# Optimization experiments

Measured on AMD Instinct MI355X. Metric: run time of the kernel, lower is better.

The kernel has to match this reference:

```python
import jax, jax.numpy as jnp
import numpy as np

B, CIN, H, W = 4, 64, 160, 160
G, K = 8, 3
KK = K * K
PAD = K // 2
CG = CIN // G  # channels per deformable group


def setup_inputs() -> dict:
    key = jax.random.key(0)
    ks = jax.random.split(key, 6)
    x = jax.random.normal(ks[0], (B, CIN, H, W), jnp.float32)
    feat = jax.random.normal(ks[1], (B, CIN, H, W), jnp.float32)
    # conv_offset weights (zero-init in the original; small random here so offsets are nontrivial)
    w_off = jax.random.normal(ks[2], (3 * G * KK, CIN, 3, 3), jnp.float32) * 0.01
    b_off = jax.random.normal(ks[3], (3 * G * KK,), jnp.float32) * 0.01
    # deformable conv weights (torchvision DeformConv2d: groups=1, bias=True)
    w_dcn = jax.random.normal(ks[4], (CIN, CIN, K, K), jnp.float32) * (1.0 / np.sqrt(CIN * KK))
    b_dcn = jax.random.normal(ks[5], (CIN,), jnp.float32) * 0.01
    return dict(x=x, feat=feat, w_off=w_off, b_off=b_off, w_dcn=w_dcn, b_dcn=b_dcn)


def _modulated_deform_conv(x, offset, mask, w, b):
    # x: [B,C,H,W]; offset: [B,2*G*KK,H,W] (interleaved dy,dx per (g,k));
    # mask: [B,G*KK,H,W]; w: [Cout,C,K,K]; stride 1, zero padding K//2.
    Bn, C, Hh, Ww = x.shape
    off = offset.reshape(Bn, G, KK, 2, Hh, Ww)
    dy = off[:, :, :, 0]  # [B,G,KK,H,W]
    dx = off[:, :, :, 1]
    ki = jnp.arange(K)
    base_y = (jnp.repeat(ki, K) - PAD).reshape(1, 1, KK, 1, 1).astype(x.dtype)
    base_x = (jnp.tile(ki, K) - PAD).reshape(1, 1, KK, 1, 1).astype(x.dtype)
    hy = jnp.arange(Hh, dtype=x.dtype).reshape(1, 1, 1, Hh, 1)
    wx = jnp.arange(Ww, dtype=x.dtype).reshape(1, 1, 1, 1, Ww)
    py = hy + base_y + dy  # sample rows  [B,G,KK,H,W]
    px = wx + base_x + dx  # sample cols
    y0 = jnp.floor(py)
    x0 = jnp.floor(px)
    ly = py - y0
    lx = px - x0
    y0i = y0.astype(jnp.int32)
    x0i = x0.astype(jnp.int32)
    xg = x.reshape(Bn, G, CG, Hh * Ww)

    def gather(yi, xi):
        valid = ((yi >= 0) & (yi < Hh) & (xi >= 0) & (xi < Ww)).astype(x.dtype)
        idx = jnp.clip(yi, 0, Hh - 1) * Ww + jnp.clip(xi, 0, Ww - 1)
        flat = idx.reshape(Bn, G, 1, KK * Hh * Ww)
        v = jnp.take_along_axis(xg, flat, axis=3).reshape(Bn, G, CG, KK, Hh, Ww)
        return v * valid[:, :, None]  # zero padding outside

    v = ((1 - ly) * (1 - lx))[:, :, None] * gather(y0i, x0i) \
      + ((1 - ly) * lx)[:, :, None] * gather(y0i, x0i + 1) \
      + (ly * (1 - lx))[:, :, None] * gather(y0i + 1, x0i) \
      + (ly * lx)[:, :, None] * gather(y0i + 1, x0i + 1)
    v = v * mask.reshape(Bn, G, 1, KK, Hh, Ww)
    wr = w.reshape(w.shape[0], G, CG, KK)
    out = jnp.einsum('ogck,bgckhw->bohw', wr, v) + b[None, :, None, None]
    return out


def reference(x, feat, w_off, b_off, w_dcn, b_dcn):
    # conv_offset: 3x3 conv, stride 1, pad 1
    out = jax.lax.conv_general_dilated(
        feat, w_off, (1, 1), ((1, 1), (1, 1)),
        dimension_numbers=('NCHW', 'OIHW', 'NCHW')) + b_off[None, :, None, None]
    o1, o2, m = jnp.split(out, 3, axis=1)
    offset = jnp.concatenate([o1, o2], axis=1)  # [B, 2*G*KK, H, W]
    mask = jax.nn.sigmoid(m)                    # [B, G*KK, H, W]
    return _modulated_deform_conv(x, offset, mask, w_dcn, b_dcn)
```

## Files before the change

kernel.cpp:

```cpp
#include <hip/hip_runtime.h>
#include <math.h>

#define Bn   4
#define CINc 64
#define Hh   160
#define Ww   160
#define Gg   8
#define HW   (Hh * Ww)
#define COFF 216

#define OROW 220
#define VROW 200
#define OFFS_SZ (64 * OROW)
#define UNION_SZ 12800

typedef short bf16x8 __attribute__((ext_vector_type(8)));
typedef float f32x4  __attribute__((ext_vector_type(4)));

static __device__ __forceinline__ unsigned short f2bf(float f) {
    unsigned int u = __float_as_uint(f);
    u = (u + 0x7fffu + ((u >> 16) & 1u)) >> 16;
    return (unsigned short)u;
}
static __device__ __forceinline__ float bf2f(unsigned short s) {
    return __uint_as_float(((unsigned int)s) << 16);
}
static __device__ __forceinline__ float blo(unsigned int u) {
    return __uint_as_float(u << 16);
}
static __device__ __forceinline__ float bhi(unsigned int u) {
    return __uint_as_float(u & 0xffff0000u);
}

#define WB 180
__global__ __launch_bounds__(256)
void prep_kernel(const float* __restrict__ feat, const float* __restrict__ x,
                 const float* __restrict__ w_off, const float* __restrict__ w_dcn,
                 unsigned short* __restrict__ featT, unsigned short* __restrict__ xG,
                 unsigned short* __restrict__ wofrag, unsigned short* __restrict__ wfrag) {
    const int blk = blockIdx.x;
    const int t = threadIdx.x;
    if (blk < 1280) {
        __shared__ float tile[CINc][161];
        const int isx = blk >= 640;
        const int rem = isx ? blk - 640 : blk;
        const int b = rem / Hh;
        const int h = rem % Hh;
        const float* src = isx ? x : feat;
        for (int i = t; i < CINc * Ww; i += 256) {
            int ci = i / Ww, w = i % Ww;
            tile[ci][w] = src[(((size_t)b * CINc + ci) * Hh + h) * Ww + w];
        }
        __syncthreads();
        if (isx) {
            for (int i = t; i < CINc * Ww; i += 256) {
                int g = i / (Ww * 8);
                int r = i % (Ww * 8);
                int w = r >> 3, cg = r & 7;
                xG[(((size_t)b * Gg + g) * HW + h * Ww + w) * 8 + cg] = f2bf(tile[g * 8 + cg][w]);
            }
        } else {
            for (int i = t; i < CINc * Ww; i += 256) {
                int w = i / CINc, ci = i % CINc;
                featT[(((size_t)b * Hh + h) * Ww + w) * CINc + ci] = f2bf(tile[ci][w]);
            }
        }
    } else {
        for (int e = (blk - 1280) * 256 + t; e < 147456 + 36864; e += WB * 256) {
            if (e < 147456) {
                const int j    = e & 7;
                const int lane = (e >> 3) & 63;
                const int rest = e >> 9;
                const int mt = rest & 15;
                const int q  = rest >> 4;
                const int ks = q & 1;
                const int kp = q >> 1;
                const int co = mt * 16 + (lane & 15);
                const int ci = ks * 32 + (lane >> 4) * 8 + j;
                float v = (co < COFF) ? w_off[(size_t)co * 576 + ci * 9 + kp] : 0.f;
                wofrag[e] = f2bf(v);
            } else {
                const int e2   = e - 147456;
                const int j    = e2 & 7;
                const int lane = (e2 >> 3) & 63;
                const int mt   = (e2 >> 9) & 3;
                const int ks   = e2 >> 11;
                const int m = mt * 16 + (lane & 15);
                const int k = ks * 32 + (lane >> 4) * 8 + j;
                const int g = k / 72, r = k % 72;
                const int kk = r >> 3, cg = r & 7;
                const int ci = g * 8 + cg;
                wfrag[e2] = f2bf(w_dcn[((size_t)m * CINc + ci) * 9 + kk]);
            }
        }
    }
}

__global__ __launch_bounds__(256, 3)
void dcnpack_fused(const unsigned short* __restrict__ featT,
                   const unsigned short* __restrict__ xG,
                   const unsigned short* __restrict__ wofrag,
                   const unsigned short* __restrict__ wfrag,
                   const float* __restrict__ b_off,
                   const float* __restrict__ b_dcn,
                   float* __restrict__ out) {
    __shared__ unsigned short smem[OFFS_SZ + UNION_SZ];
    unsigned short* offs = smem;
    unsigned short* halo = smem + OFFS_SZ;
    unsigned short* vbuf = smem + OFFS_SZ;

    const int b  = blockIdx.z;
    const int h0 = blockIdx.y * 8;
    const int w0 = blockIdx.x * 8;
    const int t  = threadIdx.x;
    const int wv   = t >> 6;
    const int lane = t & 63;
    const int n    = lane & 15;
    const int kg   = lane >> 4;

    for (int task = t; task < 800; task += 256) {
        const int pix = task >> 3, ch = task & 7;
        const int ry = pix / 10, rx = pix % 10;
        const int gh = h0 - 1 + ry, gw = w0 - 1 + rx;
        float4 v = make_float4(0.f, 0.f, 0.f, 0.f);
        if (gh >= 0 && gh < Hh && gw >= 0 && gw < Ww)
            v = *(const float4*)(featT + ((((size_t)b * Hh) + gh) * Ww + gw) * CINc + ch * 8);
        *(float4*)(halo + pix * 72 + ch * 8) = v;
    }
    __syncthreads();

    const int bbase0 = (((n >> 3) * 10) + (n & 7)) * 72 + kg * 8;

    f32x4 cacc[4][4] = {};
    #pragma unroll
    for (int s = 0; s < 18; ++s) {
        const int kp = s >> 1, ks = s & 1;
        const int ky = kp / 3, kx = kp % 3;
        bf16x8 af[4];
        #pragma unroll
        for (int i = 0; i < 4; ++i)
            af[i] = *(const bf16x8*)(wofrag +
                (((size_t)(kp * 2 + ks) * 16 + wv + 4 * i) * 64 + lane) * 8);
        #pragma unroll
        for (int nt = 0; nt < 4; ++nt) {
            const bf16x8 bfr = *(const bf16x8*)(halo + bbase0 + nt * 1440 +
                                                (ky * 10 + kx) * 72 + ks * 32);
            #pragma unroll
            for (int i = 0; i < 4; ++i)
                cacc[i][nt] = __builtin_amdgcn_mfma_f32_16x16x32_bf16(af[i], bfr, cacc[i][nt], 0, 0, 0);
        }
    }

    #pragma unroll
    for (int i = 0; i < 4; ++i) {
        const int mt = wv + 4 * i;
        #pragma unroll
        for (int r = 0; r < 4; ++r) {
            const int co = mt * 16 + kg * 4 + r;
            if (co < COFF) {
                const float bias = b_off[co];
                const int ismask = (co >= 144);
                const int gk = ismask ? (co - 144) : (co >> 1);
                const int type = ismask ? 2 : (co & 1);
                #pragma unroll
                for (int nt = 0; nt < 4; ++nt) {
                    const int p = nt * 16 + n;
                    float v = cacc[i][nt][r] + bias;
                    if (ismask) v = 1.f / (1.f + expf(-v));
                    offs[p * OROW + gk * 3 + type] = f2bf(v);
                }
            }
        }
    }
    __syncthreads();

    f32x4 dacc[4] = {};

    for (int c = 0; c < 3; ++c) {
        #pragma unroll 3
        for (int it = 0; it < 6; ++it) {
            const int task = t + it * 256;
            const int p    = task & 63;
            const int u    = c * 24 + (task >> 6);
            const int g    = u / 9;
            const int k    = u % 9;
            const int h = h0 + (p >> 3);
            const int w = w0 + (p & 7);

            const float dy   = bf2f(offs[p * OROW + u * 3 + 0]);
            const float dx   = bf2f(offs[p * OROW + u * 3 + 1]);
            const float mask = bf2f(offs[p * OROW + u * 3 + 2]);

            const float py  = (float)h + (float)(k / 3 - 1) + dy;
            const float pxx = (float)w + (float)(k % 3 - 1) + dx;
            const float y0f = floorf(py), x0f = floorf(pxx);
            const float ly = py - y0f, lx = pxx - x0f;
            const int y0 = (int)y0f, x0i = (int)x0f;
            const int y1 = y0 + 1,  x1  = x0i + 1;

            const float vy0 = (y0 >= 0 && y0 < Hh) ? 1.f : 0.f;
            const float vy1 = (y1 >= 0 && y1 < Hh) ? 1.f : 0.f;
            const float vx0 = (x0i >= 0 && x0i < Ww) ? 1.f : 0.f;
            const float vx1 = (x1 >= 0 && x1 < Ww) ? 1.f : 0.f;

            const float c00 = (1.f - ly) * (1.f - lx) * vy0 * vx0 * mask;
            const float c01 = (1.f - ly) * lx         * vy0 * vx1 * mask;
            const float c10 = ly         * (1.f - lx) * vy1 * vx0 * mask;
            const float c11 = ly         * lx         * vy1 * vx1 * mask;

            const int y0c = min(max(y0, 0), Hh - 1), y1c = min(max(y1, 0), Hh - 1);
            const int x0c = min(max(x0i, 0), Ww - 1), x1c = min(max(x1, 0), Ww - 1);

            const unsigned short* xb = xG + ((size_t)b * Gg + g) * HW * 8;
            const uint4 q00 = *(const uint4*)(xb + ((size_t)y0c * Ww + x0c) * 8);
            const uint4 q01 = *(const uint4*)(xb + ((size_t)y0c * Ww + x1c) * 8);
            const uint4 q10 = *(const uint4*)(xb + ((size_t)y1c * Ww + x0c) * 8);
            const uint4 q11 = *(const uint4*)(xb + ((size_t)y1c * Ww + x1c) * 8);
            const unsigned int a00[4] = {q00.x, q00.y, q00.z, q00.w};
            const unsigned int a01[4] = {q01.x, q01.y, q01.z, q01.w};
            const unsigned int a10[4] = {q10.x, q10.y, q10.z, q10.w};
            const unsigned int a11[4] = {q11.x, q11.y, q11.z, q11.w};

            unsigned short res[8];
            #pragma unroll
            for (int j = 0; j < 4; ++j) {
                const float vl = c00 * blo(a00[j]) + c01 * blo(a01[j])
                               + c10 * blo(a10[j]) + c11 * blo(a11[j]);
                const float vh = c00 * bhi(a00[j]) + c01 * bhi(a01[j])
                               + c10 * bhi(a10[j]) + c11 * bhi(a11[j]);
                res[2 * j]     = f2bf(vl);
                res[2 * j + 1] = f2bf(vh);
            }
            *(uint4*)(vbuf + (size_t)p * VROW + (u - c * 24) * 8) = *(const uint4*)res;
        }
        __syncthreads();

        #pragma unroll
        for (int s = 0; s < 6; ++s) {
            const int ksg = c * 6 + s;
            const bf16x8 afr = *(const bf16x8*)(wfrag + (((size_t)ksg * 4 + wv) * 64 + lane) * 8);
            #pragma unroll
            for (int nt = 0; nt < 4; ++nt) {
                const bf16x8 bfr = *(const bf16x8*)(vbuf + (nt * 16 + n) * VROW + s * 32 + kg * 8);
                dacc[nt] = __builtin_amdgcn_mfma_f32_16x16x32_bf16(afr, bfr, dacc[nt], 0, 0, 0);
            }
        }
        __syncthreads();
    }

    #pragma unroll
    for (int nt = 0; nt < 4; ++nt) {
        const int p = nt * 16 + n;
        const int h = h0 + (p >> 3);
        const int w = w0 + (p & 7);
        #pragma unroll
        for (int r = 0; r < 4; ++r) {
            const int o = wv * 16 + kg * 4 + r;
            out[(((size_t)b * CINc + o) * HW) + h * Ww + w] = dacc[nt][r] + b_dcn[o];
        }
    }
}

extern "C" void kernel_launch(void* const* d_in, const int* in_sizes, int n_in,
                              void* d_out, int out_size, void* d_ws, size_t ws_size,
                              hipStream_t stream) {
    const float* x     = (const float*)d_in[0];
    const float* feat  = (const float*)d_in[1];
    const float* w_off = (const float*)d_in[2];
    const float* b_off = (const float*)d_in[3];
    const float* w_dcn = (const float*)d_in[4];
    const float* b_dcn = (const float*)d_in[5];
    float* out = (float*)d_out;

    unsigned short* featT  = (unsigned short*)d_ws;
    unsigned short* xG     = featT + (size_t)Bn * HW * CINc;
    unsigned short* wofrag = xG + (size_t)Bn * HW * CINc;
    unsigned short* wfrag  = wofrag + (size_t)147456;

    prep_kernel<<<dim3(1280 + WB), 256, 0, stream>>>(
        feat, x, w_off, w_dcn, featT, xG, wofrag, wfrag);
    dcnpack_fused<<<dim3(Ww / 8, Hh / 8, Bn), 256, 0, stream>>>(
        featT, xG, wofrag, wfrag, b_off, b_dcn, out);
}
```

Measured before the change: 215.1 us.

## Batch gather loads, prefetch MFMA weight fragments, vectorize prep stores

The bilinear sampling stage is split into two phases. All 24 gather loads for a chunk are issued up front, then blended, with a packed bf16 convert instruction replacing the software rounding. Weight fragments for both MFMA loops are prefetched ahead of use: a triple-buffered prefetch in the offset conv and a preload before the barrier in the deform GEMM. The prep kernel uses float4 loads and packed 32-bit bf16 stores. The intent is to hide global-memory latency with more loads in flight, at the cost of much higher register pressure under a 3-blocks-per-SM launch bound, which could cause spills.

```diff
diff --git a/kernel.cpp b/kernel.cpp
--- a/kernel.cpp
+++ b/kernel.cpp
@@ -47,22 +47,30 @@
         const int b = rem / Hh;
         const int h = rem % Hh;
         const float* src = isx ? x : feat;
-        for (int i = t; i < CINc * Ww; i += 256) {
-            int ci = i / Ww, w = i % Ww;
-            tile[ci][w] = src[(((size_t)b * CINc + ci) * Hh + h) * Ww + w];
+        for (int i = t; i < CINc * (Ww / 4); i += 256) {
+            int ci = i / (Ww / 4), w4 = i % (Ww / 4);
+            float4 v = *(const float4*)(src + (((size_t)b * CINc + ci) * Hh + h) * Ww + w4 * 4);
+            tile[ci][w4 * 4 + 0] = v.x; tile[ci][w4 * 4 + 1] = v.y;
+            tile[ci][w4 * 4 + 2] = v.z; tile[ci][w4 * 4 + 3] = v.w;
         }
         __syncthreads();
         if (isx) {
-            for (int i = t; i < CINc * Ww; i += 256) {
-                int g = i / (Ww * 8);
-                int r = i % (Ww * 8);
-                int w = r >> 3, cg = r & 7;
-                xG[(((size_t)b * Gg + g) * HW + h * Ww + w) * 8 + cg] = f2bf(tile[g * 8 + cg][w]);
+            for (int i = t; i < CINc * Ww / 2; i += 256) {
+                int g = i / (Ww * 4);
+                int r = i % (Ww * 4);
+                int w = r >> 2, cp = r & 3;
+                unsigned int lo = f2bf(tile[g * 8 + 2 * cp][w]);
+                unsigned int hi = f2bf(tile[g * 8 + 2 * cp + 1][w]);
+                *(unsigned int*)(xG + (((size_t)b * Gg + g) * HW + h * Ww + w) * 8 + 2 * cp)
+                    = lo | (hi << 16);
             }
         } else {
-            for (int i = t; i < CINc * Ww; i += 256) {
-                int w = i / CINc, ci = i % CINc;
-                featT[(((size_t)b * Hh + h) * Ww + w) * CINc + ci] = f2bf(tile[ci][w]);
+            for (int i = t; i < CINc * Ww / 2; i += 256) {
+                int w = i / (CINc / 2), cp = i % (CINc / 2);
+                unsigned int lo = f2bf(tile[2 * cp][w]);
+                unsigned int hi = f2bf(tile[2 * cp + 1][w]);
+                *(unsigned int*)(featT + (((size_t)b * Hh + h) * Ww + w) * CINc + 2 * cp)
+                    = lo | (hi << 16);
             }
         }
     } else {
@@ -96,6 +104,14 @@
     }
 }
 
+#define BLEND_J(out_, w00, w01, w10, w11, c00, c01, c10, c11) {            \
+    float vl_ = (c00) * blo(w00) + (c01) * blo(w01)                        \
+              + (c10) * blo(w10) + (c11) * blo(w11);                       \
+    float vh_ = (c00) * bhi(w00) + (c01) * bhi(w01)                        \
+              + (c10) * bhi(w10) + (c11) * bhi(w11);                       \
+    asm("v_cvt_pk_bf16_f32 %0, %1, %2" : "=v"(out_) : "v"(vl_), "v"(vh_)); \
+}
+
 __global__ __launch_bounds__(256, 3)
 void dcnpack_fused(const unsigned short* __restrict__ featT,
                    const unsigned short* __restrict__ xG,
@@ -132,22 +148,31 @@
     const int bbase0 = (((n >> 3) * 10) + (n & 7)) * 72 + kg * 8;
 
     f32x4 cacc[4][4] = {};
+    bf16x8 af[3][4];
+    #pragma unroll
+    for (int i = 0; i < 4; ++i)
+        af[0][i] = *(const bf16x8*)(wofrag + (((size_t)0 * 16 + wv + 4 * i) * 64 + lane) * 8);
+    #pragma unroll
+    for (int i = 0; i < 4; ++i)
+        af[1][i] = *(const bf16x8*)(wofrag + (((size_t)1 * 16 + wv + 4 * i) * 64 + lane) * 8);
+
     #pragma unroll
     for (int s = 0; s < 18; ++s) {
+        if (s + 2 < 18) {
+            #pragma unroll
+            for (int i = 0; i < 4; ++i)
+                af[(s + 2) % 3][i] = *(const bf16x8*)(wofrag +
+                    (((size_t)(s + 2) * 16 + wv + 4 * i) * 64 + lane) * 8);
+        }
         const int kp = s >> 1, ks = s & 1;
         const int ky = kp / 3, kx = kp % 3;
-        bf16x8 af[4];
-        #pragma unroll
-        for (int i = 0; i < 4; ++i)
-            af[i] = *(const bf16x8*)(wofrag +
-                (((size_t)(kp * 2 + ks) * 16 + wv + 4 * i) * 64 + lane) * 8);
         #pragma unroll
         for (int nt = 0; nt < 4; ++nt) {
             const bf16x8 bfr = *(const bf16x8*)(halo + bbase0 + nt * 1440 +
                                                 (ky * 10 + kx) * 72 + ks * 32);
             #pragma unroll
             for (int i = 0; i < 4; ++i)
-                cacc[i][nt] = __builtin_amdgcn_mfma_f32_16x16x32_bf16(af[i], bfr, cacc[i][nt], 0, 0, 0);
+                cacc[i][nt] = __builtin_amdgcn_mfma_f32_16x16x32_bf16(af[s % 3][i], bfr, cacc[i][nt], 0, 0, 0);
         }
     }
 
@@ -175,24 +200,25 @@
     __syncthreads();
 
     f32x4 dacc[4] = {};
+    const int p_t = t & 63;
+    const int h_s = h0 + (p_t >> 3);
+    const int w_s = w0 + (p_t & 7);
 
     for (int c = 0; c < 3; ++c) {
-        #pragma unroll 3
+        float cf[6][4];
+        uint4 q[6][4];
+        #pragma unroll
         for (int it = 0; it < 6; ++it) {
-            const int task = t + it * 256;
-            const int p    = task & 63;
-            const int u    = c * 24 + (task >> 6);
-            const int g    = u / 9;
-            const int k    = u % 9;
-            const int h = h0 + (p >> 3);
-            const int w = w0 + (p & 7);
-
-            const float dy   = bf2f(offs[p * OROW + u * 3 + 0]);
-            const float dx   = bf2f(offs[p * OROW + u * 3 + 1]);
-            const float mask = bf2f(offs[p * OROW + u * 3 + 2]);
-
-            const float py  = (float)h + (float)(k / 3 - 1) + dy;
-            const float pxx = (float)w + (float)(k % 3 - 1) + dx;
+            const int u = c * 24 + wv + it * 4;
+            const int g = u / 9;
+            const int k = u % 9;
+
+            const float dy   = bf2f(offs[p_t * OROW + u * 3 + 0]);
+            const float dx   = bf2f(offs[p_t * OROW + u * 3 + 1]);
+            const float mask = bf2f(offs[p_t * OROW + u * 3 + 2]);
+
+            const float py  = (float)h_s + (float)(k / 3 - 1) + dy;
+            const float pxx = (float)w_s + (float)(k % 3 - 1) + dx;
             const float y0f = floorf(py), x0f = floorf(pxx);
             const float ly = py - y0f, lx = pxx - x0f;
             const int y0 = (int)y0f, x0i = (int)x0f;
@@ -203,46 +229,49 @@
             const float vx0 = (x0i >= 0 && x0i < Ww) ? 1.f : 0.f;
             const float vx1 = (x1 >= 0 && x1 < Ww) ? 1.f : 0.f;
 
-            const float c00 = (1.f - ly) * (1.f - lx) * vy0 * vx0 * mask;
-            const float c01 = (1.f - ly) * lx         * vy0 * vx1 * mask;
-            const float c10 = ly         * (1.f - lx) * vy1 * vx0 * mask;
-            const float c11 = ly         * lx         * vy1 * vx1 * mask;
+            cf[it][0] = (1.f - ly) * (1.f - lx) * vy0 * vx0 * mask;
+            cf[it][1] = (1.f - ly) * lx         * vy0 * vx1 * mask;
+            cf[it][2] = ly         * (1.f - lx) * vy1 * vx0 * mask;
+            cf[it][3] = ly         * lx         * vy1 * vx1 * mask;
 
             const int y0c = min(max(y0, 0), Hh - 1), y1c = min(max(y1, 0), Hh - 1);
             const int x0c = min(max(x0i, 0), Ww - 1), x1c = min(max(x1, 0), Ww - 1);
 
             const unsigned short* xb = xG + ((size_t)b * Gg + g) * HW * 8;
-            const uint4 q00 = *(const uint4*)(xb + ((size_t)y0c * Ww + x0c) * 8);
-            const uint4 q01 = *(const uint4*)(xb + ((size_t)y0c * Ww + x1c) * 8);
-            const uint4 q10 = *(const uint4*)(xb + ((size_t)y1c * Ww + x0c) * 8);
-            const uint4 q11 = *(const uint4*)(xb + ((size_t)y1c * Ww + x1c) * 8);
-            const unsigned int a00[4] = {q00.x, q00.y, q00.z, q00.w};
-            const unsigned int a01[4] = {q01.x, q01.y, q01.z, q01.w};
-            const unsigned int a10[4] = {q10.x, q10.y, q10.z, q10.w};
-            const unsigned int a11[4] = {q11.x, q11.y, q11.z, q11.w};
-
-            unsigned short res[8];
-            #pragma unroll
-            for (int j = 0; j < 4; ++j) {
-                const float vl = c00 * blo(a00[j]) + c01 * blo(a01[j])
-                               + c10 * blo(a10[j]) + c11 * blo(a11[j]);
-                const float vh = c00 * bhi(a00[j]) + c01 * bhi(a01[j])
-                               + c10 * bhi(a10[j]) + c11 * bhi(a11[j]);
-                res[2 * j]     = f2bf(vl);
-                res[2 * j + 1] = f2bf(vh);
-            }
-            *(uint4*)(vbuf + (size_t)p * VROW + (u - c * 24) * 8) = *(const uint4*)res;
-        }
+            q[it][0] = *(const uint4*)(xb + ((size_t)y0c * Ww + x0c) * 8);
+            q[it][1] = *(const uint4*)(xb + ((size_t)y0c * Ww + x1c) * 8);
+            q[it][2] = *(const uint4*)(xb + ((size_t)y1c * Ww + x0c) * 8);
+            q[it][3] = *(const uint4*)(xb + ((size_t)y1c * Ww + x1c) * 8);
+        }
+
+        #pragma unroll
+        for (int it = 0; it < 6; ++it) {
+            unsigned int rr0, rr1, rr2, rr3;
+            BLEND_J(rr0, q[it][0].x, q[it][1].x, q[it][2].x, q[it][3].x,
+                    cf[it][0], cf[it][1], cf[it][2], cf[it][3]);
+            BLEND_J(rr1, q[it][0].y, q[it][1].y, q[it][2].y, q[it][3].y,
+                    cf[it][0], cf[it][1], cf[it][2], cf[it][3]);
+            BLEND_J(rr2, q[it][0].z, q[it][1].z, q[it][2].z, q[it][3].z,
+                    cf[it][0], cf[it][1], cf[it][2], cf[it][3]);
+            BLEND_J(rr3, q[it][0].w, q[it][1].w, q[it][2].w, q[it][3].w,
+                    cf[it][0], cf[it][1], cf[it][2], cf[it][3]);
+            uint4 res; res.x = rr0; res.y = rr1; res.z = rr2; res.w = rr3;
+            *(uint4*)(vbuf + (size_t)p_t * VROW + (wv + it * 4) * 8) = res;
+        }
+
+        bf16x8 afr[6];
+        #pragma unroll
+        for (int s = 0; s < 6; ++s)
+            afr[s] = *(const bf16x8*)(wfrag + (((size_t)(c * 6 + s) * 4 + wv) * 64 + lane) * 8);
+
         __syncthreads();
 
         #pragma unroll
         for (int s = 0; s < 6; ++s) {
-            const int ksg = c * 6 + s;
-            const bf16x8 afr = *(const bf16x8*)(wfrag + (((size_t)ksg * 4 + wv) * 64 + lane) * 8);
             #pragma unroll
             for (int nt = 0; nt < 4; ++nt) {
                 const bf16x8 bfr = *(const bf16x8*)(vbuf + (nt * 16 + n) * VROW + s * 32 + kg * 8);
-                dacc[nt] = __builtin_amdgcn_mfma_f32_16x16x32_bf16(afr, bfr, dacc[nt], 0, 0, 0);
+                dacc[nt] = __builtin_amdgcn_mfma_f32_16x16x32_bf16(afr[s], bfr, dacc[nt], 0, 0, 0);
             }
         }
         __syncthreads();
```

After: 192.3 us. -10.6%, faster.
